# Kernel tuning notes

Hardware: AMD Instinct MI355X
Metric: run time of the kernel (lower is better)

Reference implementation:

```python
import jax
import jax.numpy as jnp
from jax import lax
import numpy as np

D_MODEL = 768
D_INNER = 1536  # d_model * expand_factor
D_STATE = 16
D_CONV = 4
BATCH = 2
SEQ = 2048
EPS = 1e-5


def silu(x):
    return x * jax.nn.sigmoid(x)


def setup_inputs() -> dict:
    key = jax.random.key(0)
    ks = jax.random.split(key, 24)
    n = lambda k, shape, s=0.1: jax.random.normal(k, shape, dtype=jnp.float32) * s
    inp = {
        "x": jax.random.normal(ks[0], (BATCH, SEQ, D_MODEL), dtype=jnp.float32),
        "ln_g": jnp.ones((D_MODEL,), jnp.float32),
        "ln_b": jnp.zeros((D_MODEL,), jnp.float32),
        "W_in": n(ks[1], (D_INNER, D_MODEL)),
        "b_in": n(ks[2], (D_INNER,)),
        "conv_w": n(ks[3], (D_INNER, 1, D_CONV), 0.02),
        "conv_b": jnp.zeros((D_INNER,), jnp.float32),
        "W_A": n(ks[4], (D_STATE, D_INNER)),
        "b_A": n(ks[5], (D_STATE,)),
        "W_B": n(ks[6], (D_STATE, D_INNER)),
        "b_B": n(ks[7], (D_STATE,)),
        "W_C": n(ks[8], (D_STATE, D_INNER)),
        "b_C": n(ks[9], (D_STATE,)),
        "W_dt": n(ks[10], (D_STATE, D_INNER)),
        "b_dt": n(ks[11], (D_STATE,)),
        "W_S": n(ks[12], (2 * D_INNER, D_INNER)),
        "b_S": n(ks[13], (2 * D_INNER,)),
        "W_gate": n(ks[14], (D_INNER, D_MODEL)),
        "b_gate": n(ks[15], (D_INNER,)),
        "W_out": n(ks[16], (D_MODEL, D_INNER)),
        "b_out": n(ks[17], (D_MODEL,)),
    }
    return inp


def reference(x, ln_g, ln_b, W_in, b_in, conv_w, conv_b, W_A, b_A, W_B, b_B,
              W_C, b_C, W_dt, b_dt, W_S, b_S, W_gate, b_gate, W_out, b_out):
    residual = x
    # LayerNorm
    mu = jnp.mean(x, axis=-1, keepdims=True)
    var = jnp.mean((x - mu) ** 2, axis=-1, keepdims=True)
    xn = (x - mu) * lax.rsqrt(var + EPS) * ln_g + ln_b
    # in projection -> [B, S, D_INNER]
    xp = xn @ W_in.T + b_in
    # depthwise causal conv1d over time
    k = conv_w.shape[-1]
    xc = jnp.moveaxis(xp, 1, 2)  # [B, D, L]
    xc = lax.conv_general_dilated(
        xc, conv_w, window_strides=(1,), padding=[(k - 1, 0)],
        dimension_numbers=("NCH", "OIH", "NCH"),
        feature_group_count=xc.shape[1])
    xc = xc + conv_b[None, :, None]
    xa = silu(jnp.moveaxis(xc, 1, 2))  # [B, S, D]
    # selective gating of SSM input (S_b computed but unused, as in source)
    S = xa @ W_S.T + b_S
    d = xa.shape[-1]
    S_a = jax.nn.sigmoid(S[..., :d])
    u = xa * S_a  # [B, S, D]
    # input-dependent SSM params [B, S, N]
    A = -jnp.exp(u @ W_A.T + b_A)
    dt = jnp.exp(u @ W_dt.T + b_dt)
    Bm = u @ W_B.T + b_B
    Cm = u @ W_C.T + b_C
    decay = jnp.exp(A * dt)  # [B, S, N]

    def step(h, inputs):
        dec_t, B_t, C_t, u_t = inputs  # [B,N],[B,N],[B,N],[B,D]
        h = h * dec_t[:, None, :] + B_t[:, None, :] * u_t[:, :, None]  # [B,D,N]
        y = jnp.einsum("bdn,bn->bd", h, C_t)
        return h, y

    h0 = jnp.zeros((u.shape[0], u.shape[2], decay.shape[-1]), u.dtype)
    scan_in = (jnp.moveaxis(decay, 1, 0), jnp.moveaxis(Bm, 1, 0),
               jnp.moveaxis(Cm, 1, 0), jnp.moveaxis(u, 1, 0))
    _, ys = lax.scan(step, h0, scan_in)
    y = jnp.moveaxis(ys, 0, 1)  # [B, S, D]
    # output gating + projection + residual
    gate = silu(xn @ W_gate.T + b_gate)
    out = (gate * y) @ W_out.T + b_out + residual
    return out
```

## Files before the change

kernel.cpp:

```cpp
#include <hip/hip_runtime.h>


typedef unsigned short u16;
using short8 = __attribute__((ext_vector_type(8))) short;
using f32x4  = __attribute__((ext_vector_type(4))) float;

#define BATCH 2
#define SEQ   2048
#define DM    768
#define DI    1536
#define NIG   (2*DI)
#define NST   16
#define LCH   64
#define NCH   32
#define NTOK  (BATCH*SEQ)

__device__ __forceinline__ u16 f2b(float x) {
  unsigned u = __float_as_uint(x);
  u += 0x7FFFu + ((u >> 16) & 1u);
  return (u16)(u >> 16);
}
__device__ __forceinline__ float b2f(u16 v) { return __uint_as_float((unsigned)v << 16); }
__device__ __forceinline__ float sigmoidf_(float x) { return 1.f / (1.f + expf(-x)); }
__device__ __forceinline__ float siluf_(float x) { return x / (1.f + expf(-x)); }

__global__ __launch_bounds__(256) void cast_bf16(const float* __restrict__ in, u16* __restrict__ out, int n4) {
  int i = blockIdx.x * 256 + threadIdx.x;
  if (i >= n4) return;
  float4 v = ((const float4*)in)[i];
  ushort4 o; o.x = f2b(v.x); o.y = f2b(v.y); o.z = f2b(v.z); o.w = f2b(v.w);
  ((ushort4*)out)[i] = o;
}

__global__ __launch_bounds__(256) void cast_ingate(const float* __restrict__ Wi, const float* __restrict__ Wg,
                                                   const float* __restrict__ bi, const float* __restrict__ bg,
                                                   u16* __restrict__ Wb, float* __restrict__ bias) {
  int i = blockIdx.x * 256 + threadIdx.x;
  if (i >= NIG * DM) return;
  int r = i / DM, c = i % DM;
  Wb[i] = f2b(r < DI ? Wi[(size_t)r * DM + c] : Wg[(size_t)(r - DI) * DM + c]);
  if (i < NIG) bias[i] = (i < DI) ? bi[i] : bg[i - DI];
}

__global__ __launch_bounds__(256) void cast_wabcd(const float* __restrict__ WA, const float* __restrict__ Wdt,
                                                  const float* __restrict__ WB, const float* __restrict__ WC,
                                                  const float* __restrict__ bA, const float* __restrict__ bdt,
                                                  const float* __restrict__ bB, const float* __restrict__ bC,
                                                  u16* __restrict__ Wb, float* __restrict__ bias64) {
  int i = blockIdx.x * 256 + threadIdx.x;
  if (i >= 64 * DI) return;
  int r = i / DI, c = i % DI;
  const float* src = (r < 16) ? WA + (size_t)r * DI
                  : (r < 32) ? Wdt + (size_t)(r - 16) * DI
                  : (r < 48) ? WB + (size_t)(r - 32) * DI
                             : WC + (size_t)(r - 48) * DI;
  Wb[i] = f2b(src[c]);
  if (i < 64) bias64[i] = (i < 16) ? bA[i] : (i < 32) ? bdt[i - 16] : (i < 48) ? bB[i - 32] : bC[i - 48];
}

__global__ __launch_bounds__(256) void ln_kernel(const float* __restrict__ x, const float* __restrict__ g,
                                                 const float* __restrict__ bb, u16* __restrict__ xn) {
  int m = blockIdx.x, tid = threadIdx.x;
  const float* xr = x + (size_t)m * DM;
  float v0 = xr[tid], v1 = xr[tid + 256], v2 = xr[tid + 512];
  float s  = v0 + v1 + v2;
  float s2 = fmaf(v0, v0, fmaf(v1, v1, v2 * v2));
  #pragma unroll
  for (int off = 32; off > 0; off >>= 1) { s += __shfl_down(s, off); s2 += __shfl_down(s2, off); }
  __shared__ float sh[8];
  int wave = tid >> 6, lane = tid & 63;
  if (lane == 0) { sh[wave] = s; sh[4 + wave] = s2; }
  __syncthreads();
  float S1 = sh[0] + sh[1] + sh[2] + sh[3];
  float S2 = sh[4] + sh[5] + sh[6] + sh[7];
  float mu = S1 * (1.f / DM);
  float var = S2 * (1.f / DM) - mu * mu;
  float rs = rsqrtf(var + 1e-5f);
  u16* o = xn + (size_t)m * DM;
  o[tid]       = f2b((v0 - mu) * rs * g[tid]       + bb[tid]);
  o[tid + 256] = f2b((v1 - mu) * rs * g[tid + 256] + bb[tid + 256]);
  o[tid + 512] = f2b((v2 - mu) * rs * g[tid + 512] + bb[tid + 512]);
}

__device__ __forceinline__ void gll16(const void* g, void* l) {
  __builtin_amdgcn_global_load_lds((const __attribute__((address_space(1))) void*)g,
                                   (__attribute__((address_space(3))) void*)l, 16, 0, 0);
}

template <int MODE>
__global__ __launch_bounds__(512) void gemm_bt(const u16* __restrict__ A, const u16* __restrict__ B,
                                               const float* __restrict__ bias, const float* __restrict__ aux,
                                               const u16* __restrict__ auxb,
                                               float* __restrict__ C, u16* __restrict__ Cb,
                                               int M, int N, int K) {
  __shared__ __align__(16) u16 As[2][128 * 32];
  __shared__ __align__(16) u16 Bs[2][128 * 32];
  const int tid = threadIdx.x, wave = tid >> 6, lane = tid & 63;

  const int nbx = gridDim.x, nwg = nbx * gridDim.y;
  const int orig = blockIdx.y * nbx + blockIdx.x;
  const int cpx = nwg >> 3;
  const int swz = (orig & 7) * cpx + (orig >> 3);
  const int m0 = (swz / nbx) * 128, n0 = (swz % nbx) * 128;

  const int wm = (wave >> 1) * 32, wn = (wave & 1) * 64;
  const int fr = lane & 15, fq = lane >> 4;
  f32x4 acc[2][4] = {};

  const int c0 = tid;
  const u16* Ag0 = A + (size_t)(m0 + (c0 >> 2)) * K + ((c0 & 3) ^ ((c0 >> 3) & 3)) * 8;
  const u16* Bg0 = B + (size_t)(n0 + (c0 >> 2)) * K + ((c0 & 3) ^ ((c0 >> 3) & 3)) * 8;
  const int lofs = (wave * 64) * 8;

  int offA[2], offB[4];
  #pragma unroll
  for (int i = 0; i < 2; ++i) {
    int ra = wm + i * 16 + fr;
    offA[i] = ra * 32 + (fq ^ ((ra >> 1) & 3)) * 8;
  }
  #pragma unroll
  for (int i = 0; i < 4; ++i) {
    int rb = wn + i * 16 + fr;
    offB[i] = rb * 32 + (fq ^ ((rb >> 1) & 3)) * 8;
  }

  const int nk = K >> 5;
  gll16(Ag0, (u16*)As[0] + lofs);
  gll16(Bg0, (u16*)Bs[0] + lofs);

  for (int t = 0; t < nk; ++t) {
    __syncthreads();
    if (t + 1 < nk) {
      gll16(Ag0 + (t + 1) * 32, (u16*)As[(t + 1) & 1] + lofs);
      gll16(Bg0 + (t + 1) * 32, (u16*)Bs[(t + 1) & 1] + lofs);
    }
    const u16* as = As[t & 1];
    const u16* bs = Bs[t & 1];
    short8 av[2], bv[4];
    #pragma unroll
    for (int i = 0; i < 2; ++i) av[i] = *(const short8*)(as + offA[i]);
    #pragma unroll
    for (int i = 0; i < 4; ++i) bv[i] = *(const short8*)(bs + offB[i]);
    #pragma unroll
    for (int mi = 0; mi < 2; ++mi)
      #pragma unroll
      for (int ni = 0; ni < 4; ++ni)
        acc[mi][ni] = __builtin_amdgcn_mfma_f32_16x16x32_bf16(av[mi], bv[ni], acc[mi][ni], 0, 0, 0);
  }

  #pragma unroll
  for (int ni = 0; ni < 4; ++ni) {
    int col = n0 + wn + ni * 16 + fr;
    float bv_ = bias[col];
    #pragma unroll
    for (int mi = 0; mi < 2; ++mi) {
      int row = m0 + wm + mi * 16 + fq * 4;
      #pragma unroll
      for (int j = 0; j < 4; ++j) {
        size_t off = (size_t)(row + j) * N + col;
        float z = acc[mi][ni][j] + bv_;
        if (MODE == 0) {
          C[off] = z + aux[off];
        } else if (MODE == 1) {
          Cb[off] = f2b(b2f(auxb[off]) * sigmoidf_(z));
        } else {
          Cb[off] = f2b(z);
        }
      }
    }
  }
}

__global__ __launch_bounds__(256) void gemm_abcd(const u16* __restrict__ A, const u16* __restrict__ B,
                                                 const float* __restrict__ bias64,
                                                 float* __restrict__ dec, float* __restrict__ Bm,
                                                 float* __restrict__ Cm, int M, int K) {
  __shared__ __align__(16) u16 As[2][64 * 64];
  __shared__ __align__(16) u16 Bs[2][64 * 64];
  const int tid = threadIdx.x, wave = tid >> 6, lane = tid & 63;
  const int m0 = blockIdx.x * 64;
  const int wm = wave * 16;
  const int fr = lane & 15, fq = lane >> 4;
  f32x4 acc[4] = {};

  const int c0 = tid, c1 = tid + 256;
  const u16* Ag0 = A + (size_t)(m0 + (c0 >> 3)) * K + ((c0 & 7) ^ ((c0 >> 3) & 7)) * 8;
  const u16* Ag1 = A + (size_t)(m0 + (c1 >> 3)) * K + ((c1 & 7) ^ ((c1 >> 3) & 7)) * 8;
  const u16* Bg0 = B + (size_t)(c0 >> 3) * K + ((c0 & 7) ^ ((c0 >> 3) & 7)) * 8;
  const u16* Bg1 = B + (size_t)(c1 >> 3) * K + ((c1 & 7) ^ ((c1 >> 3) & 7)) * 8;
  const int lo0 = (wave * 64) * 8;
  const int lo1 = (256 + wave * 64) * 8;

  int offAv[2], offBv[2][4];
  {
    int r = wm + fr;
    #pragma unroll
    for (int kk = 0; kk < 2; ++kk) offAv[kk] = r * 64 + ((kk * 4 + fq) ^ (r & 7)) * 8;
    #pragma unroll
    for (int i = 0; i < 4; ++i) {
      int rb = i * 16 + fr;
      #pragma unroll
      for (int kk = 0; kk < 2; ++kk) offBv[kk][i] = rb * 64 + ((kk * 4 + fq) ^ (rb & 7)) * 8;
    }
  }

  const int nk = K >> 6;
  gll16(Ag0, (u16*)As[0] + lo0);
  gll16(Ag1, (u16*)As[0] + lo1);
  gll16(Bg0, (u16*)Bs[0] + lo0);
  gll16(Bg1, (u16*)Bs[0] + lo1);

  for (int t = 0; t < nk; ++t) {
    __syncthreads();
    if (t + 1 < nk) {
      int ko = (t + 1) * 64;
      gll16(Ag0 + ko, (u16*)As[(t + 1) & 1] + lo0);
      gll16(Ag1 + ko, (u16*)As[(t + 1) & 1] + lo1);
      gll16(Bg0 + ko, (u16*)Bs[(t + 1) & 1] + lo0);
      gll16(Bg1 + ko, (u16*)Bs[(t + 1) & 1] + lo1);
    }
    const u16* as = As[t & 1];
    const u16* bs = Bs[t & 1];
    #pragma unroll
    for (int kk = 0; kk < 2; ++kk) {
      short8 av = *(const short8*)(as + offAv[kk]);
      short8 bv[4];
      #pragma unroll
      for (int i = 0; i < 4; ++i) bv[i] = *(const short8*)(bs + offBv[kk][i]);
      #pragma unroll
      for (int ni = 0; ni < 4; ++ni)
        acc[ni] = __builtin_amdgcn_mfma_f32_16x16x32_bf16(av, bv[ni], acc[ni], 0, 0, 0);
    }
  }

  float bA_ = bias64[fr], bDt_ = bias64[16 + fr], bB_ = bias64[32 + fr], bC_ = bias64[48 + fr];
  #pragma unroll
  for (int j = 0; j < 4; ++j) {
    int row = m0 + wm + fq * 4 + j;
    size_t o = (size_t)row * NST + fr;
    float zA = acc[0][j] + bA_, zDt = acc[1][j] + bDt_;
    dec[o] = expf(-expf(zA + zDt));
    Bm[o]  = acc[2][j] + bB_;
    Cm[o]  = acc[3][j] + bC_;
  }
}

__global__ __launch_bounds__(256) void conv_silu(const u16* __restrict__ xpg, const float* __restrict__ cw,
                                                 const float* __restrict__ cb, u16* __restrict__ xab) {
  int idx = blockIdx.x * 256 + threadIdx.x;
  int d = idx % DI;
  int token = idx / DI;
  int t = token % SEQ;
  size_t base = (size_t)token * NIG + d;
  float4 w = ((const float4*)cw)[d];
  float acc = cb[d];
  if (t >= 3) acc = fmaf(b2f(xpg[base - 3 * NIG]), w.x, acc);
  if (t >= 2) acc = fmaf(b2f(xpg[base - 2 * NIG]), w.y, acc);
  if (t >= 1) acc = fmaf(b2f(xpg[base - 1 * NIG]), w.z, acc);
  acc = fmaf(b2f(xpg[base]), w.w, acc);
  xab[idx] = f2b(siluf_(acc));
}

__global__ __launch_bounds__(256) void scan_phase1(const u16* __restrict__ ub, const float* __restrict__ dec,
                                                   const float* __restrict__ Bm, float* __restrict__ lend,
                                                   float* __restrict__ P) {
  __shared__ float dl[LCH * NST], bl[LCH * NST];
  int bid = blockIdx.x;
  int dblk = bid % 6, b = (bid / 6) % BATCH, c = bid / (6 * BATCH);
  int d = dblk * 256 + threadIdx.x;
  int t0 = c * LCH;
  size_t base16 = (size_t)(b * SEQ + t0) * NST;
  for (int i = threadIdx.x; i < LCH * NST; i += 256) { dl[i] = dec[base16 + i]; bl[i] = Bm[base16 + i]; }
  __syncthreads();
  float h[NST];
  #pragma unroll
  for (int n = 0; n < NST; ++n) h[n] = 0.f;
  const u16* up = ub + (size_t)(b * SEQ + t0) * DI + d;
  for (int t = 0; t < LCH; ++t) {
    float uu = b2f(up[(size_t)t * DI]);
    #pragma unroll
    for (int n = 0; n < NST; ++n) h[n] = fmaf(h[n], dl[t * NST + n], bl[t * NST + n] * uu);
  }
  float* lo = lend + ((size_t)(c * BATCH + b) * DI + d) * NST;
  ((float4*)lo)[0] = make_float4(h[0], h[1], h[2], h[3]);
  ((float4*)lo)[1] = make_float4(h[4], h[5], h[6], h[7]);
  ((float4*)lo)[2] = make_float4(h[8], h[9], h[10], h[11]);
  ((float4*)lo)[3] = make_float4(h[12], h[13], h[14], h[15]);
  if (dblk == 0 && threadIdx.x < NST) {
    float pr = 1.f;
    for (int t = 0; t < LCH; ++t) pr *= dl[t * NST + threadIdx.x];
    P[(size_t)(c * BATCH + b) * NST + threadIdx.x] = pr;
  }
}

__global__ __launch_bounds__(256) void scan_phase2(const float* __restrict__ lend, const float* __restrict__ P,
                                                   float* __restrict__ Hin) {
  int flat = blockIdx.x * 256 + threadIdx.x;
  int n = flat & 15;
  int d = (flat >> 4) % DI;
  int b = flat / (DI * NST);
  float h = 0.f;
  for (int c = 0; c < NCH; ++c) {
    size_t idx = ((size_t)(c * BATCH + b) * DI + d) * NST + n;
    Hin[idx] = h;
    h = fmaf(P[(size_t)(c * BATCH + b) * NST + n], h, lend[idx]);
  }
}

__global__ __launch_bounds__(256) void scan_phase3(const u16* __restrict__ ub, const float* __restrict__ dec,
                                                   const float* __restrict__ Bm, const float* __restrict__ Cm,
                                                   const float* __restrict__ Hin, const u16* __restrict__ xpg,
                                                   u16* __restrict__ gy) {
  __shared__ float dl[LCH * NST], bl[LCH * NST], cl[LCH * NST];
  int bid = blockIdx.x;
  int dblk = bid % 6, b = (bid / 6) % BATCH, c = bid / (6 * BATCH);
  int d = dblk * 256 + threadIdx.x;
  int t0 = c * LCH;
  size_t base16 = (size_t)(b * SEQ + t0) * NST;
  for (int i = threadIdx.x; i < LCH * NST; i += 256) {
    dl[i] = dec[base16 + i]; bl[i] = Bm[base16 + i]; cl[i] = Cm[base16 + i];
  }
  __syncthreads();
  float h[NST];
  const float4* hi = (const float4*)(Hin + ((size_t)(c * BATCH + b) * DI + d) * NST);
  float4 h0 = hi[0], h1 = hi[1], h2 = hi[2], h3 = hi[3];
  h[0]=h0.x; h[1]=h0.y; h[2]=h0.z; h[3]=h0.w; h[4]=h1.x; h[5]=h1.y; h[6]=h1.z; h[7]=h1.w;
  h[8]=h2.x; h[9]=h2.y; h[10]=h2.z; h[11]=h2.w; h[12]=h3.x; h[13]=h3.y; h[14]=h3.z; h[15]=h3.w;
  const u16* up = ub + (size_t)(b * SEQ + t0) * DI + d;
  const u16* gp = xpg + (size_t)(b * SEQ + t0) * NIG + DI + d;
  u16* yp = gy + (size_t)(b * SEQ + t0) * DI + d;
  for (int t = 0; t < LCH; ++t) {
    float uu = b2f(up[(size_t)t * DI]);
    float acc = 0.f;
    #pragma unroll
    for (int n = 0; n < NST; ++n) {
      h[n] = fmaf(h[n], dl[t * NST + n], bl[t * NST + n] * uu);
      acc = fmaf(h[n], cl[t * NST + n], acc);
    }
    float g = b2f(gp[(size_t)t * NIG]);
    yp[(size_t)t * DI] = f2b(siluf_(g) * acc);
  }
}

extern "C" void kernel_launch(void* const* d_in, const int* in_sizes, int n_in,
                              void* d_out, int out_size, void* d_ws, size_t ws_size,
                              hipStream_t stream) {
  const float* x      = (const float*)d_in[0];
  const float* ln_g   = (const float*)d_in[1];
  const float* ln_b   = (const float*)d_in[2];
  const float* W_in   = (const float*)d_in[3];
  const float* b_in   = (const float*)d_in[4];
  const float* conv_w = (const float*)d_in[5];
  const float* conv_b = (const float*)d_in[6];
  const float* W_A    = (const float*)d_in[7];
  const float* b_A    = (const float*)d_in[8];
  const float* W_B    = (const float*)d_in[9];
  const float* b_B    = (const float*)d_in[10];
  const float* W_C    = (const float*)d_in[11];
  const float* b_C    = (const float*)d_in[12];
  const float* W_dt   = (const float*)d_in[13];
  const float* b_dt   = (const float*)d_in[14];
  const float* W_S    = (const float*)d_in[15];
  const float* b_S    = (const float*)d_in[16];
  const float* W_gate = (const float*)d_in[17];
  const float* b_gate = (const float*)d_in[18];
  const float* W_out  = (const float*)d_in[19];
  const float* b_out  = (const float*)d_in[20];
  float* out = (float*)d_out;

  char* p = (char*)d_ws;
  auto alloc = [&](size_t bytes) { char* r = p; p += (bytes + 255) & ~(size_t)255; return r; };
  u16*   Wigb    = (u16*)alloc((size_t)NIG * DM * 2);
  float* biasig  = (float*)alloc((size_t)NIG * 4);
  u16*   WSb     = (u16*)alloc((size_t)DI * DI * 2);
  u16*   Woutb   = (u16*)alloc((size_t)DM * DI * 2);
  u16*   Wabcd   = (u16*)alloc((size_t)64 * DI * 2);
  float* bias64  = (float*)alloc(64 * 4);
  u16*   xnb     = (u16*)alloc((size_t)NTOK * DM * 2);
  u16*   xpg     = (u16*)alloc((size_t)NTOK * NIG * 2);
  u16*   xab     = (u16*)alloc((size_t)NTOK * DI * 2);
  u16*   ub      = (u16*)alloc((size_t)NTOK * DI * 2);
  float* decb    = (float*)alloc((size_t)NTOK * NST * 4);
  float* Bmb     = (float*)alloc((size_t)NTOK * NST * 4);
  float* Cmb     = (float*)alloc((size_t)NTOK * NST * 4);
  float* lend    = (float*)alloc((size_t)NCH * BATCH * DI * NST * 4);
  float* Hin     = (float*)alloc((size_t)NCH * BATCH * DI * NST * 4);
  float* P       = (float*)alloc((size_t)NCH * BATCH * NST * 4);
  u16* gy = xab;

  cast_ingate<<<(NIG * DM + 255) / 256, 256, 0, stream>>>(W_in, W_gate, b_in, b_gate, Wigb, biasig);
  cast_bf16<<<(DI * DI / 4 + 255) / 256, 256, 0, stream>>>(W_S, WSb, DI * DI / 4);
  cast_bf16<<<(DM * DI / 4 + 255) / 256, 256, 0, stream>>>(W_out, Woutb, DM * DI / 4);
  cast_wabcd<<<(64 * DI + 255) / 256, 256, 0, stream>>>(W_A, W_dt, W_B, W_C, b_A, b_dt, b_B, b_C, Wabcd, bias64);

  ln_kernel<<<NTOK, 256, 0, stream>>>(x, ln_g, ln_b, xnb);

  gemm_bt<2><<<dim3(NIG / 128, NTOK / 128), 512, 0, stream>>>(xnb, Wigb, biasig, nullptr, nullptr,
                                                              nullptr, xpg, NTOK, NIG, DM);

  conv_silu<<<NTOK * DI / 256, 256, 0, stream>>>(xpg, conv_w, conv_b, xab);

  gemm_bt<1><<<dim3(DI / 128, NTOK / 128), 512, 0, stream>>>(xab, WSb, b_S, nullptr, xab,
                                                             nullptr, ub, NTOK, DI, DI);

  gemm_abcd<<<NTOK / 64, 256, 0, stream>>>(ub, Wabcd, bias64, decb, Bmb, Cmb, NTOK, DI);

  scan_phase1<<<NCH * BATCH * (DI / 256), 256, 0, stream>>>(ub, decb, Bmb, lend, P);
  scan_phase2<<<BATCH * DI * NST / 256, 256, 0, stream>>>(lend, P, Hin);
  scan_phase3<<<NCH * BATCH * (DI / 256), 256, 0, stream>>>(ub, decb, Bmb, Cmb, Hin, xpg, gy);

  gemm_bt<0><<<dim3(DM / 128, NTOK / 128), 512, 0, stream>>>(gy, Woutb, b_out, x, nullptr,
                                                             out, nullptr, NTOK, DM, DI);
}
```

Baseline: 225.4 us.

## Deepen GEMM pipeline, split-K the ABCD projection, vectorize conv_silu

The main bf16 GEMM moves from double to quad buffering, using explicit vmcnt waits and raw barriers so three tile loads stay in flight. The small ABCD projection, previously launched with only 64 blocks, is split four ways along K, and a new combine kernel applies the bias and exponentials. conv_silu now processes 8 channels per thread with 16-byte vector loads and stores. In exchange, the GEMM uses more LDS, which may reduce occupancy, and the split-K path adds a launch and a partial-sum buffer.

```diff
diff --git a/kernel.cpp b/kernel.cpp
--- a/kernel.cpp
+++ b/kernel.cpp
@@ -93,8 +93,8 @@
                                                const u16* __restrict__ auxb,
                                                float* __restrict__ C, u16* __restrict__ Cb,
                                                int M, int N, int K) {
-  __shared__ __align__(16) u16 As[2][128 * 32];
-  __shared__ __align__(16) u16 Bs[2][128 * 32];
+  __shared__ __align__(16) u16 As[4][128 * 32];
+  __shared__ __align__(16) u16 Bs[4][128 * 32];
   const int tid = threadIdx.x, wave = tid >> 6, lane = tid & 63;
 
   const int nbx = gridDim.x, nwg = nbx * gridDim.y;
@@ -125,28 +125,36 @@
   }
 
   const int nk = K >> 5;
-  gll16(Ag0, (u16*)As[0] + lofs);
-  gll16(Bg0, (u16*)Bs[0] + lofs);
-
-  for (int t = 0; t < nk; ++t) {
-    __syncthreads();
-    if (t + 1 < nk) {
-      gll16(Ag0 + (t + 1) * 32, (u16*)As[(t + 1) & 1] + lofs);
-      gll16(Bg0 + (t + 1) * 32, (u16*)Bs[(t + 1) & 1] + lofs);
-    }
-    const u16* as = As[t & 1];
-    const u16* bs = Bs[t & 1];
-    short8 av[2], bv[4];
-    #pragma unroll
-    for (int i = 0; i < 2; ++i) av[i] = *(const short8*)(as + offA[i]);
-    #pragma unroll
-    for (int i = 0; i < 4; ++i) bv[i] = *(const short8*)(bs + offB[i]);
-    #pragma unroll
-    for (int mi = 0; mi < 2; ++mi)
-      #pragma unroll
-      for (int ni = 0; ni < 4; ++ni)
-        acc[mi][ni] = __builtin_amdgcn_mfma_f32_16x16x32_bf16(av[mi], bv[ni], acc[mi][ni], 0, 0, 0);
-  }
+
+#define STAGE_BT(tt) { gll16(Ag0 + (tt) * 32, (u16*)As[(tt) & 3] + lofs); \
+                       gll16(Bg0 + (tt) * 32, (u16*)Bs[(tt) & 3] + lofs); }
+#define COMPUTE_BT(tt) { const u16* as_ = As[(tt) & 3]; const u16* bs_ = Bs[(tt) & 3]; \
+    short8 av[2], bv[4]; \
+    _Pragma("unroll") for (int i = 0; i < 2; ++i) av[i] = *(const short8*)(as_ + offA[i]); \
+    _Pragma("unroll") for (int i = 0; i < 4; ++i) bv[i] = *(const short8*)(bs_ + offB[i]); \
+    _Pragma("unroll") for (int mi = 0; mi < 2; ++mi) \
+      _Pragma("unroll") for (int ni = 0; ni < 4; ++ni) \
+        acc[mi][ni] = __builtin_amdgcn_mfma_f32_16x16x32_bf16(av[mi], bv[ni], acc[mi][ni], 0, 0, 0); }
+
+  STAGE_BT(0); STAGE_BT(1); STAGE_BT(2);
+
+  for (int t = 0; t < nk - 3; ++t) {
+    asm volatile("s_waitcnt vmcnt(4)" ::: "memory");
+    __builtin_amdgcn_s_barrier();
+    STAGE_BT(t + 3);
+    COMPUTE_BT(t);
+  }
+  asm volatile("s_waitcnt vmcnt(4)" ::: "memory");
+  __builtin_amdgcn_s_barrier();
+  COMPUTE_BT(nk - 3);
+  asm volatile("s_waitcnt vmcnt(2)" ::: "memory");
+  __builtin_amdgcn_s_barrier();
+  COMPUTE_BT(nk - 2);
+  asm volatile("s_waitcnt vmcnt(0)" ::: "memory");
+  __builtin_amdgcn_s_barrier();
+  COMPUTE_BT(nk - 1);
+#undef STAGE_BT
+#undef COMPUTE_BT
 
   #pragma unroll
   for (int ni = 0; ni < 4; ++ni) {
@@ -172,22 +180,23 @@
 }
 
 __global__ __launch_bounds__(256) void gemm_abcd(const u16* __restrict__ A, const u16* __restrict__ B,
-                                                 const float* __restrict__ bias64,
-                                                 float* __restrict__ dec, float* __restrict__ Bm,
-                                                 float* __restrict__ Cm, int M, int K) {
+                                                 float* __restrict__ Zp, int M, int K) {
   __shared__ __align__(16) u16 As[2][64 * 64];
   __shared__ __align__(16) u16 Bs[2][64 * 64];
   const int tid = threadIdx.x, wave = tid >> 6, lane = tid & 63;
   const int m0 = blockIdx.x * 64;
+  const int ks = blockIdx.y;
+  const int Kq = K >> 2;
+  const int kbase = ks * Kq;
   const int wm = wave * 16;
   const int fr = lane & 15, fq = lane >> 4;
   f32x4 acc[4] = {};
 
   const int c0 = tid, c1 = tid + 256;
-  const u16* Ag0 = A + (size_t)(m0 + (c0 >> 3)) * K + ((c0 & 7) ^ ((c0 >> 3) & 7)) * 8;
-  const u16* Ag1 = A + (size_t)(m0 + (c1 >> 3)) * K + ((c1 & 7) ^ ((c1 >> 3) & 7)) * 8;
-  const u16* Bg0 = B + (size_t)(c0 >> 3) * K + ((c0 & 7) ^ ((c0 >> 3) & 7)) * 8;
-  const u16* Bg1 = B + (size_t)(c1 >> 3) * K + ((c1 & 7) ^ ((c1 >> 3) & 7)) * 8;
+  const u16* Ag0 = A + (size_t)(m0 + (c0 >> 3)) * K + kbase + ((c0 & 7) ^ ((c0 >> 3) & 7)) * 8;
+  const u16* Ag1 = A + (size_t)(m0 + (c1 >> 3)) * K + kbase + ((c1 & 7) ^ ((c1 >> 3) & 7)) * 8;
+  const u16* Bg0 = B + (size_t)(c0 >> 3) * K + kbase + ((c0 & 7) ^ ((c0 >> 3) & 7)) * 8;
+  const u16* Bg1 = B + (size_t)(c1 >> 3) * K + kbase + ((c1 & 7) ^ ((c1 >> 3) & 7)) * 8;
   const int lo0 = (wave * 64) * 8;
   const int lo1 = (256 + wave * 64) * 8;
 
@@ -204,7 +213,7 @@
     }
   }
 
-  const int nk = K >> 6;
+  const int nk = Kq >> 6;
   gll16(Ag0, (u16*)As[0] + lo0);
   gll16(Ag1, (u16*)As[0] + lo1);
   gll16(Bg0, (u16*)Bs[0] + lo0);
@@ -233,32 +242,63 @@
     }
   }
 
-  float bA_ = bias64[fr], bDt_ = bias64[16 + fr], bB_ = bias64[32 + fr], bC_ = bias64[48 + fr];
-  #pragma unroll
-  for (int j = 0; j < 4; ++j) {
-    int row = m0 + wm + fq * 4 + j;
-    size_t o = (size_t)row * NST + fr;
-    float zA = acc[0][j] + bA_, zDt = acc[1][j] + bDt_;
-    dec[o] = expf(-expf(zA + zDt));
-    Bm[o]  = acc[2][j] + bB_;
-    Cm[o]  = acc[3][j] + bC_;
-  }
+  float* zp = Zp + (size_t)ks * M * 64;
+  #pragma unroll
+  for (int ni = 0; ni < 4; ++ni) {
+    int col = ni * 16 + fr;
+    #pragma unroll
+    for (int j = 0; j < 4; ++j) {
+      int row = m0 + wm + fq * 4 + j;
+      zp[(size_t)row * 64 + col] = acc[ni][j];
+    }
+  }
+}
+
+__global__ __launch_bounds__(256) void abcd_combine(const float* __restrict__ Zp, const float* __restrict__ bias64,
+                                                    float* __restrict__ dec, float* __restrict__ Bm,
+                                                    float* __restrict__ Cm, int M) {
+  int idx = blockIdx.x * 256 + threadIdx.x;
+  int row = idx >> 4, n = idx & 15;
+  float zA = bias64[n], zDt = bias64[16 + n], zB = bias64[32 + n], zC = bias64[48 + n];
+  #pragma unroll
+  for (int ks = 0; ks < 4; ++ks) {
+    const float* zp = Zp + ((size_t)ks * M + row) * 64;
+    zA += zp[n]; zDt += zp[16 + n]; zB += zp[32 + n]; zC += zp[48 + n];
+  }
+  size_t o = (size_t)row * NST + n;
+  dec[o] = expf(-expf(zA + zDt));
+  Bm[o] = zB;
+  Cm[o] = zC;
 }
 
 __global__ __launch_bounds__(256) void conv_silu(const u16* __restrict__ xpg, const float* __restrict__ cw,
                                                  const float* __restrict__ cb, u16* __restrict__ xab) {
   int idx = blockIdx.x * 256 + threadIdx.x;
-  int d = idx % DI;
-  int token = idx / DI;
+  int d8 = idx % (DI / 8);
+  int token = idx / (DI / 8);
   int t = token % SEQ;
-  size_t base = (size_t)token * NIG + d;
-  float4 w = ((const float4*)cw)[d];
-  float acc = cb[d];
-  if (t >= 3) acc = fmaf(b2f(xpg[base - 3 * NIG]), w.x, acc);
-  if (t >= 2) acc = fmaf(b2f(xpg[base - 2 * NIG]), w.y, acc);
-  if (t >= 1) acc = fmaf(b2f(xpg[base - 1 * NIG]), w.z, acc);
-  acc = fmaf(b2f(xpg[base]), w.w, acc);
-  xab[idx] = f2b(siluf_(acc));
+  int d0 = d8 * 8;
+  const short8* xv = (const short8*)(xpg + (size_t)token * NIG + d0);
+  short8 z8 = {0, 0, 0, 0, 0, 0, 0, 0};
+  short8 x3 = (t >= 3) ? xv[-3 * (NIG / 8)] : z8;
+  short8 x2 = (t >= 2) ? xv[-2 * (NIG / 8)] : z8;
+  short8 x1 = (t >= 1) ? xv[-1 * (NIG / 8)] : z8;
+  short8 x0 = xv[0];
+  const float4* cw4 = (const float4*)cw;
+  float4 cbl = ((const float4*)cb)[d8 * 2], cbh = ((const float4*)cb)[d8 * 2 + 1];
+  float cbv[8] = {cbl.x, cbl.y, cbl.z, cbl.w, cbh.x, cbh.y, cbh.z, cbh.w};
+  short8 o;
+  #pragma unroll
+  for (int j = 0; j < 8; ++j) {
+    float4 w = cw4[d0 + j];
+    float a = cbv[j];
+    a = fmaf(b2f((u16)x3[j]), w.x, a);
+    a = fmaf(b2f((u16)x2[j]), w.y, a);
+    a = fmaf(b2f((u16)x1[j]), w.z, a);
+    a = fmaf(b2f((u16)x0[j]), w.w, a);
+    o[j] = (short)f2b(siluf_(a));
+  }
+  *(short8*)(xab + (size_t)token * DI + d0) = o;
 }
 
 __global__ __launch_bounds__(256) void scan_phase1(const u16* __restrict__ ub, const float* __restrict__ dec,
@@ -380,6 +420,7 @@
   u16*   xpg     = (u16*)alloc((size_t)NTOK * NIG * 2);
   u16*   xab     = (u16*)alloc((size_t)NTOK * DI * 2);
   u16*   ub      = (u16*)alloc((size_t)NTOK * DI * 2);
+  float* Zp      = (float*)alloc((size_t)4 * NTOK * 64 * 4);
   float* decb    = (float*)alloc((size_t)NTOK * NST * 4);
   float* Bmb     = (float*)alloc((size_t)NTOK * NST * 4);
   float* Cmb     = (float*)alloc((size_t)NTOK * NST * 4);
@@ -398,12 +439,13 @@
   gemm_bt<2><<<dim3(NIG / 128, NTOK / 128), 512, 0, stream>>>(xnb, Wigb, biasig, nullptr, nullptr,
                                                               nullptr, xpg, NTOK, NIG, DM);
 
-  conv_silu<<<NTOK * DI / 256, 256, 0, stream>>>(xpg, conv_w, conv_b, xab);
+  conv_silu<<<NTOK * (DI / 8) / 256, 256, 0, stream>>>(xpg, conv_w, conv_b, xab);
 
   gemm_bt<1><<<dim3(DI / 128, NTOK / 128), 512, 0, stream>>>(xab, WSb, b_S, nullptr, xab,
                                                              nullptr, ub, NTOK, DI, DI);
 
-  gemm_abcd<<<NTOK / 64, 256, 0, stream>>>(ub, Wabcd, bias64, decb, Bmb, Cmb, NTOK, DI);
+  gemm_abcd<<<dim3(NTOK / 64, 4), 256, 0, stream>>>(ub, Wabcd, Zp, NTOK, DI);
+  abcd_combine<<<NTOK * 16 / 256, 256, 0, stream>>>(Zp, bias64, decb, Bmb, Cmb, NTOK);
 
   scan_phase1<<<NCH * BATCH * (DI / 256), 256, 0, stream>>>(ub, decb, Bmb, lend, P);
   scan_phase2<<<BATCH * DI * NST / 256, 256, 0, stream>>>(lend, P, Hin);
```

Result: faster. 206.0 us (-8.6%).
